# Kernel tuning notes

Hardware: AMD Instinct MI355X
Metric: run time of the kernel (lower is better)

## Reference

```python
import jax, jax.numpy as jnp
import numpy as np

N_NODES = 100000
N_EDGES = 3200000
N_GRAPHS = 64
EPS = 1e-5


def setup_inputs() -> dict:
    key = jax.random.key(0)
    ks = jax.random.split(key, 14)
    x = jax.random.normal(ks[0], (N_NODES, 3), dtype=jnp.float32)
    edge_index = jax.random.randint(ks[1], (2, N_EDGES), 0, N_NODES, dtype=jnp.int32)
    edge_attr = jax.random.uniform(ks[2], (N_EDGES, 2), dtype=jnp.float32)
    batch = jnp.sort(jax.random.randint(ks[3], (N_NODES,), 0, N_GRAPHS, dtype=jnp.int32))
    # SplineConv weights: [K=4 kernels, C_in, C_out]
    W1 = jax.random.normal(ks[4], (4, 3, 8), dtype=jnp.float32) * 0.4
    W2 = jax.random.normal(ks[5], (4, 8, 16), dtype=jnp.float32) * 0.25
    W3 = jax.random.normal(ks[6], (4, 16, 32), dtype=jnp.float32) * 0.2
    g1 = jnp.ones((8,), jnp.float32); b1 = jnp.zeros((8,), jnp.float32)
    g2 = jnp.ones((16,), jnp.float32); b2 = jnp.zeros((16,), jnp.float32)
    g3 = jnp.ones((32,), jnp.float32); b3 = jnp.zeros((32,), jnp.float32)
    fc_w = jax.random.normal(ks[7], (10, 32), dtype=jnp.float32) * 0.15  # Linear(32,10,bias=False)
    return dict(x=x, edge_index=edge_index, edge_attr=edge_attr, batch=batch,
                W1=W1, W2=W2, W3=W3, g1=g1, b1=b1, g2=g2, b2=b2, g3=g3, b3=b3,
                fc_w=fc_w)


def _basis(edge_attr):
    # degree-1 open B-spline, kernel_size=2 per dim, dim=2 -> 4 fixed kernel indices
    u = jnp.clip(edge_attr, 0.0, 1.0)
    u0, u1 = u[:, 0], u[:, 1]
    return jnp.stack([(1 - u0) * (1 - u1),  # kernel (0,0)
                      u0 * (1 - u1),        # kernel (1,0)
                      (1 - u0) * u1,        # kernel (0,1)
                      u0 * u1], axis=-1)    # kernel (1,1)  -> [E,4]


def _spline_conv(x, src, dst, basis, W, inv_deg):
    # gather source feats, basis-weighted kernel mix, scatter-mean to targets
    msg = jnp.einsum('ek,ec,kcd->ed', basis, x[src], W)  # [E, C_out]
    agg = jax.ops.segment_sum(msg, dst, num_segments=x.shape[0])
    return agg * inv_deg


def _bn(x, g, b):
    mu = jnp.mean(x, axis=0)
    var = jnp.mean((x - mu) ** 2, axis=0)  # biased, training-mode BatchNorm
    return (x - mu) * jax.lax.rsqrt(var + EPS) * g + b


def reference(x, edge_index, edge_attr, batch, W1, W2, W3, g1, b1, g2, b2, g3, b3, fc_w):
    src, dst = edge_index[0], edge_index[1]
    B = _basis(edge_attr)
    n = x.shape[0]
    deg = jax.ops.segment_sum(jnp.ones((src.shape[0],), x.dtype), dst, num_segments=n)
    inv_deg = (1.0 / jnp.maximum(deg, 1.0))[:, None]

    h = _bn(jax.nn.elu(_spline_conv(x, src, dst, B, W1, inv_deg)), g1, b1)
    h = _bn(jax.nn.elu(_spline_conv(h, src, dst, B, W2, inv_deg)), g2, b2)
    h = _bn(jax.nn.elu(_spline_conv(h, src, dst, B, W3, inv_deg)), g3, b3)

    pooled = jax.ops.segment_sum(h, batch, num_segments=N_GRAPHS)
    cnt = jax.ops.segment_sum(jnp.ones((n,), h.dtype), batch, num_segments=N_GRAPHS)
    pooled = pooled / jnp.maximum(cnt, 1.0)[:, None]  # global_mean_pool -> [G, 32]
    return pooled @ fc_w.T  # [G, 10]
```

## Files before the change

### kernel.cpp

```cpp
#include <hip/hip_runtime.h>
#include <hip/hip_fp16.h>

#define N_NODES 100000
#define N_EDGES 3200000
#define N_GRAPHS 64
constexpr int NC    = 196;
constexpr int PBLK  = 256;
constexpr int CHUNK = N_EDGES / PBLK;
constexpr int NBLK  = (N_NODES + 255) / 256;
constexpr int LBLK  = N_NODES / 32;
constexpr int FCAP  = 18432;
constexpr int ECAP  = 2048;
#define EPS 1e-5f

typedef float f2 __attribute__((ext_vector_type(2)));
static __device__ __forceinline__ f2 mkf2(float a, float b) { f2 r; r.x = a; r.y = b; return r; }
static __device__ __forceinline__ unsigned h2u(__half2 v) { unsigned r; __builtin_memcpy(&r, &v, 4); return r; }

constexpr size_t OFF_BNS1   = 0x400;
constexpr size_t OFF_BNS2   = 0x500;
constexpr size_t OFF_BNS3   = 0x700;
constexpr size_t OFF_POOLED = 0x1000;
constexpr size_t ZERO_BYTES = 0x3000;
constexpr size_t OFF_CBASE  = 0x4000;
constexpr size_t OFF_BTOT   = 0x5000;
constexpr size_t OFF_ROWPTR = 0x10000;
constexpr size_t OFF_HISTM  = 0x80000;
constexpr size_t OFF_XP     = 0x100000;
constexpr size_t OFF_ES     = 0x200000;
constexpr size_t OFF_EP     = 0x1B00000;
constexpr size_t OFF_T1     = 0x3400000;
constexpr size_t OFF_T2     = 0x3800000;
constexpr size_t OFF_T3     = 0x4000000;

__global__ __launch_bounds__(256) void xpad_kernel(const float* __restrict__ x,
                                                   __half* __restrict__ xp) {
    int n = blockIdx.x * 256 + threadIdx.x;
    if (n >= N_NODES) return;
    __half2 a = __floats2half2_rn(x[n * 3 + 0], x[n * 3 + 1]);
    __half2 b = __floats2half2_rn(x[n * 3 + 2], 0.f);
    *(uint2*)(xp + (size_t)n * 4) = make_uint2(h2u(a), h2u(b));
}

__global__ __launch_bounds__(1024) void k_hist(const int* __restrict__ dst,
                                               int* __restrict__ histM) {
    __shared__ int h[NC];
    for (int i = threadIdx.x; i < NC; i += 1024) h[i] = 0;
    __syncthreads();
    int base = blockIdx.x * CHUNK;
    for (int i = threadIdx.x; i < CHUNK; i += 1024)
        atomicAdd(&h[dst[base + i] >> 9], 1);
    __syncthreads();
    for (int i = threadIdx.x; i < NC; i += 1024)
        histM[i * PBLK + blockIdx.x] = h[i];
}

__global__ __launch_bounds__(256) void k_scan1(int* __restrict__ histM,
                                               int* __restrict__ btot) {
    __shared__ int sd[256];
    int b = blockIdx.x, t = threadIdx.x;
    int v = histM[b * PBLK + t];
    sd[t] = v;
    __syncthreads();
    for (int off = 1; off < 256; off <<= 1) {
        int x = (t >= off) ? sd[t - off] : 0;
        __syncthreads();
        sd[t] += x;
        __syncthreads();
    }
    histM[b * PBLK + t] = sd[t] - v;
    if (t == 255) btot[b] = sd[255];
}

__global__ __launch_bounds__(256) void k_scan2(const int* __restrict__ btot,
                                               int* __restrict__ cbase) {
    __shared__ int sd[256];
    int t = threadIdx.x;
    int v = (t < NC) ? btot[t] : 0;
    sd[t] = v;
    __syncthreads();
    for (int off = 1; off < 256; off <<= 1) {
        int x = (t >= off) ? sd[t - off] : 0;
        __syncthreads();
        sd[t] += x;
        __syncthreads();
    }
    if (t < NC) cbase[t] = sd[t] - v;
    if (t == 0) cbase[NC] = N_EDGES;
}

__global__ __launch_bounds__(1024) void k_part(const int* __restrict__ src,
                                               const int* __restrict__ dst,
                                               const float2* __restrict__ ea,
                                               const int* __restrict__ histM,
                                               const int* __restrict__ cbase,
                                               uint2* __restrict__ Es) {
    __shared__ int cur[NC];
    for (int i = threadIdx.x; i < NC; i += 1024)
        cur[i] = cbase[i] + histM[i * PBLK + blockIdx.x];
    __syncthreads();
    int base = blockIdx.x * CHUNK;
    for (int i = threadIdx.x; i < CHUNK; i += 1024) {
        int e = base + i;
        int d = dst[e];
        float2 u = ea[e];
        float u0 = fminf(fmaxf(u.x, 0.f), 1.f);
        float u1 = fminf(fmaxf(u.y, 0.f), 1.f);
        unsigned u0q = __float2uint_rn(u0 * 524287.f);
        unsigned u1q = __float2uint_rn(u1 * 524287.f);
        unsigned w0 = (unsigned)src[e] | ((u0q & 0x7FFFu) << 17);
        unsigned w1 = (u0q >> 15) | (u1q << 4) | ((unsigned)(d & 511) << 23);
        int pos = atomicAdd(&cur[d >> 9], 1);
        Es[pos] = make_uint2(w0, w1);
    }
}

__global__ __launch_bounds__(1024) void k_fine(const uint2* __restrict__ Es,
                                               const int* __restrict__ cbase,
                                               int* __restrict__ rowptr,
                                               uint2* __restrict__ Ep) {
    extern __shared__ uint2 rec[];
    __shared__ int cnt[512];
    __shared__ int cur[512];
    __shared__ int sd[512];
    int b = blockIdx.x, t = threadIdx.x;
    int lo = cbase[b], hi = cbase[b + 1];
    int m = hi - lo;
    if (t < 512) cnt[t] = 0;
    __syncthreads();
    for (int i = lo + t; i < hi; i += 1024)
        atomicAdd(&cnt[Es[i].y >> 23], 1);
    __syncthreads();
    if (t < 512) sd[t] = cnt[t];
    __syncthreads();
    for (int off = 1; off < 512; off <<= 1) {
        int x = (t < 512 && t >= off) ? sd[t - off] : 0;
        __syncthreads();
        if (t < 512) sd[t] += x;
        __syncthreads();
    }
    if (t < 512) {
        int excl = sd[t] - cnt[t];
        cur[t] = excl;
        int n = b * 512 + t;
        if (n < N_NODES) rowptr[n] = lo + excl;
    }
    if (b == NC - 1 && t == 0) rowptr[N_NODES] = N_EDGES;
    __syncthreads();
    if (m <= FCAP) {
        for (int i = lo + t; i < hi; i += 1024) {
            uint2 r = Es[i];
            int pos = atomicAdd(&cur[r.y >> 23], 1);
            rec[pos] = r;
        }
        __syncthreads();
        for (int i = t; i < m; i += 1024)
            Ep[lo + i] = rec[i];
    } else {
        for (int i = lo + t; i < hi; i += 1024) {
            uint2 r = Es[i];
            int pos = atomicAdd(&cur[r.y >> 23], 1);
            Ep[lo + pos] = r;
        }
    }
}

#define DECODE_EDGE(r)                                              \
    int s = r.x & 0x1FFFF;                                          \
    unsigned u0q = (r.x >> 17) | ((r.y & 0xFu) << 15);              \
    unsigned u1q = (r.y >> 4) & 0x7FFFFu;                           \
    float u0 = u0q * (1.f / 524287.f);                              \
    float u1 = u1q * (1.f / 524287.f);                              \
    float nu0 = 1.f - u0, nu1 = 1.f - u1;                           \
    float b0 = nu0 * nu1, b1 = u0 * nu1, b2 = nu0 * u1, b3 = u0 * u1;

#define L1_BODY                                                     \
        DECODE_EDGE(r)                                              \
        uint2 hv = *(const uint2*)(xp + (size_t)s * 4);             \
        float2 p0 = __half22float2(*(__half2*)&hv.x);               \
        float2 p1 = __half22float2(*(__half2*)&hv.y);               \
        float x0 = p0.x, x1 = p0.y, x2 = p1.x;                      \
        z[0] += b0 * x0; z[1]  += b0 * x1; z[2]  += b0 * x2;        \
        z[3] += b1 * x0; z[4]  += b1 * x1; z[5]  += b1 * x2;        \
        z[6] += b2 * x0; z[7]  += b2 * x1; z[8]  += b2 * x2;        \
        z[9] += b3 * x0; z[10] += b3 * x1; z[11] += b3 * x2;

__global__ __launch_bounds__(256) void layer1_kernel(const __half* __restrict__ xp,
                                                     const int* __restrict__ rowptr,
                                                     const uint2* __restrict__ Ep,
                                                     const float* __restrict__ W,
                                                     __half* __restrict__ tout) {
    __shared__ float Wl[96];
    __shared__ uint2 recL[ECAP];
    for (int i = threadIdx.x; i < 96; i += 256) Wl[i] = W[i];
    int nb = blockIdx.x * 32;
    int eb = rowptr[nb], ee = rowptr[nb + 32];
    int mm = ee - eb;
    if (mm <= ECAP)
        for (int i = threadIdx.x; i < mm; i += 256) recL[i] = Ep[eb + i];
    __syncthreads();
    int lane8 = threadIdx.x & 7;
    int n = nb + (threadIdx.x >> 3);
    int e0 = rowptr[n], e1 = rowptr[n + 1];
    float z[12];
#pragma unroll
    for (int i = 0; i < 12; ++i) z[i] = 0.f;
    if (mm <= ECAP) {
#pragma unroll 4
        for (int j = e0 - eb + lane8, je = e1 - eb; j < je; j += 8) {
            uint2 r = recL[j];
            L1_BODY
        }
    } else {
#pragma unroll 2
        for (int j = e0 + lane8; j < e1; j += 8) {
            uint2 r = Ep[j];
            L1_BODY
        }
    }
#pragma unroll
    for (int i = 0; i < 12; ++i) {
        z[i] += __shfl_xor(z[i], 4);
        z[i] += __shfl_xor(z[i], 2);
        z[i] += __shfl_xor(z[i], 1);
    }
    float y = 0.f;
#pragma unroll
    for (int kc = 0; kc < 12; ++kc) y += z[kc] * Wl[kc * 8 + lane8];
    float invd = 1.f / fmaxf((float)(e1 - e0), 1.f);
    float v = y * invd;
    v = v > 0.f ? v : expm1f(v);
    tout[(size_t)n * 8 + lane8] = __float2half_rn(v);
}

#define L2_BODY                                                     \
        DECODE_EDGE(r)                                              \
        uint2 hv = *(const uint2*)(xin + (size_t)s * 8 + 4 * ch);   \
        float2 p0 = __half22float2(*(__half2*)&hv.x);               \
        float2 p1 = __half22float2(*(__half2*)&hv.y);               \
        f2 x01 = mkf2(p0.x, p0.y), x23 = mkf2(p1.x, p1.y);          \
        S[0] += b0; S[1] += b1; S[2] += b2; S[3] += b3;             \
        f2 bbv;                                                     \
        bbv = mkf2(b0, b0); zf[0] += bbv * x01; zf[1] += bbv * x23; \
        bbv = mkf2(b1, b1); zf[2] += bbv * x01; zf[3] += bbv * x23; \
        bbv = mkf2(b2, b2); zf[4] += bbv * x01; zf[5] += bbv * x23; \
        bbv = mkf2(b3, b3); zf[6] += bbv * x01; zf[7] += bbv * x23;

__global__ __launch_bounds__(256) void layer2_kernel(const __half* __restrict__ xin,
                                                     const float* __restrict__ bns,
                                                     const float* __restrict__ g,
                                                     const float* __restrict__ bb,
                                                     const int* __restrict__ rowptr,
                                                     const uint2* __restrict__ Ep,
                                                     const float* __restrict__ W,
                                                     __half* __restrict__ tout) {
    __shared__ float scA[8], shA[8];
    __shared__ float4 Wl[140];
    __shared__ float shW[64];
    __shared__ uint2 recL[ECAP];
    int t = threadIdx.x;
    if (t < 8) {
        float mu = bns[t] * (1.f / N_NODES);
        float var = fmaxf(bns[8 + t] * (1.f / N_NODES) - mu * mu, 0.f);
        float s = g[t] * rsqrtf(var + EPS);
        scA[t] = s;
        shA[t] = bb[t] - mu * s;
    }
    int nb = blockIdx.x * 32;
    int eb = rowptr[nb], ee = rowptr[nb + 32];
    int mm = ee - eb;
    if (mm <= ECAP)
        for (int i = t; i < mm; i += 256) recL[i] = Ep[eb + i];
    __syncthreads();
    if (t < 128) {
        int k = t >> 5, d4 = (t >> 3) & 3, c = t & 7;
        float4 w = ((const float4*)W)[(k * 8 + c) * 4 + d4];
        float s = scA[c];
        Wl[k * 35 + d4 * 9 + c] = make_float4(w.x * s, w.y * s, w.z * s, w.w * s);
    } else if (t < 192) {
        int j = t - 128;
        int k = j >> 4, d = j & 15;
        float acc = 0.f;
#pragma unroll
        for (int c = 0; c < 8; ++c) acc += shA[c] * W[(k * 8 + c) * 16 + d];
        shW[j] = acc;
    }
    __syncthreads();

    int lane8 = t & 7;
    int kq = lane8 & 3, h = lane8 >> 2;
    int ch = kq & 1;
    int eo = lane8 >> 1;
    int n = nb + (t >> 3);
    int e0 = rowptr[n], e1 = rowptr[n + 1];
    f2 zf[8];
    float S[4];
#pragma unroll
    for (int i = 0; i < 8; ++i) zf[i] = mkf2(0.f, 0.f);
#pragma unroll
    for (int i = 0; i < 4; ++i) S[i] = 0.f;
    if (mm <= ECAP) {
#pragma unroll 4
        for (int j = e0 - eb + eo, je = e1 - eb; j < je; j += 4) {
            uint2 r = recL[j];
            L2_BODY
        }
    } else {
#pragma unroll 2
        for (int j = e0 + eo; j < e1; j += 4) {
            uint2 r = Ep[j];
            L2_BODY
        }
    }
#pragma unroll
    for (int i = 0; i < 8; ++i) {
        zf[i].x += __shfl_xor(zf[i].x, 4); zf[i].y += __shfl_xor(zf[i].y, 4);
        zf[i].x += __shfl_xor(zf[i].x, 2); zf[i].y += __shfl_xor(zf[i].y, 2);
    }
#pragma unroll
    for (int i = 0; i < 4; ++i) { S[i] += __shfl_xor(S[i], 4); S[i] += __shfl_xor(S[i], 2); }

    int laneW = 18 * h + 4 * ch;
    f2 ya[2], yb[2];
#pragma unroll
    for (int i = 0; i < 2; ++i) { ya[i] = mkf2(0.f, 0.f); yb[i] = mkf2(0.f, 0.f); }
#pragma unroll
    for (int k = 0; k < 4; ++k) {
        float zs[4] = {zf[2 * k].x, zf[2 * k].y, zf[2 * k + 1].x, zf[2 * k + 1].y};
#pragma unroll
        for (int i = 0; i < 4; ++i) {
            f2 zsp = mkf2(zs[i], zs[i]);
            int base = k * 35 + i + laneW;
#pragma unroll
            for (int d4 = 0; d4 < 2; ++d4) {
                float4 w = Wl[base + 9 * d4];
                ya[d4] += zsp * mkf2(w.x, w.y);
                yb[d4] += zsp * mkf2(w.z, w.w);
            }
        }
    }
    float y[8];
#pragma unroll
    for (int d4 = 0; d4 < 2; ++d4) {
        y[4 * d4 + 0] = ya[d4].x; y[4 * d4 + 1] = ya[d4].y;
        y[4 * d4 + 2] = yb[d4].x; y[4 * d4 + 3] = yb[d4].y;
    }
    float y1[4];
#pragma unroll
    for (int i = 0; i < 4; ++i) {
        float a = y[i]     + __shfl_xor(y[i],     1);
        float b = y[4 + i] + __shfl_xor(y[4 + i], 1);
        y1[i] = ch ? b : a;
    }
    int qb = (kq >> 1) & 1;
    float f0 = qb ? y1[2] : y1[0];
    float f1 = qb ? y1[3] : y1[1];
    int d = h * 8 + ch * 4 + qb * 2;
    f0 += S[0] * shW[d]     + S[1] * shW[16 + d]     + S[2] * shW[32 + d]     + S[3] * shW[48 + d];
    f1 += S[0] * shW[d + 1] + S[1] * shW[16 + d + 1] + S[2] * shW[32 + d + 1] + S[3] * shW[48 + d + 1];
    float invd = 1.f / fmaxf((float)(e1 - e0), 1.f);
    f0 *= invd; f1 *= invd;
    f0 = f0 > 0.f ? f0 : expm1f(f0);
    f1 = f1 > 0.f ? f1 : expm1f(f1);
    *(__half2*)(tout + (size_t)n * 16 + d) = __floats2half2_rn(f0, f1);
}

#define L3_BODY                                                     \
        DECODE_EDGE(r)                                              \
        uint2 hv = *(const uint2*)(xin + (size_t)s * 16 + 4 * kq);  \
        float2 p0 = __half22float2(*(__half2*)&hv.x);               \
        float2 p1 = __half22float2(*(__half2*)&hv.y);               \
        f2 x01 = mkf2(p0.x, p0.y), x23 = mkf2(p1.x, p1.y);          \
        S[0] += b0; S[1] += b1; S[2] += b2; S[3] += b3;             \
        f2 bbv;                                                     \
        bbv = mkf2(b0, b0); zf[0] += bbv * x01; zf[1] += bbv * x23; \
        bbv = mkf2(b1, b1); zf[2] += bbv * x01; zf[3] += bbv * x23; \
        bbv = mkf2(b2, b2); zf[4] += bbv * x01; zf[5] += bbv * x23; \
        bbv = mkf2(b3, b3); zf[6] += bbv * x01; zf[7] += bbv * x23;

__global__ __launch_bounds__(256) void layer3_kernel(const __half* __restrict__ xin,
                                                     const float* __restrict__ bns,
                                                     const float* __restrict__ g,
                                                     const float* __restrict__ bb,
                                                     const int* __restrict__ rowptr,
                                                     const uint2* __restrict__ Ep,
                                                     const float* __restrict__ W,
                                                     __half* __restrict__ tout) {
    __shared__ float scA[16], shA[16];
    __shared__ float4 Wl[580];
    __shared__ float shW[128];
    __shared__ uint2 recL[ECAP];
    int t = threadIdx.x;
    if (t < 16) {
        float mu = bns[t] * (1.f / N_NODES);
        float var = fmaxf(bns[16 + t] * (1.f / N_NODES) - mu * mu, 0.f);
        float s = g[t] * rsqrtf(var + EPS);
        scA[t] = s;
        shA[t] = bb[t] - mu * s;
    }
    int nb = blockIdx.x * 32;
    int eb = rowptr[nb], ee = rowptr[nb + 32];
    int mm = ee - eb;
    if (mm <= ECAP)
        for (int i = t; i < mm; i += 256) recL[i] = Ep[eb + i];
    __syncthreads();
    for (int i = t; i < 512; i += 256) {
        int k = i >> 7, d4 = (i >> 4) & 7, c = i & 15;
        float4 w = ((const float4*)W)[(k * 16 + c) * 8 + d4];
        float s = scA[c];
        Wl[k * 145 + d4 * 18 + (d4 >> 2) + c + 2 * (c >> 3)] =
            make_float4(w.x * s, w.y * s, w.z * s, w.w * s);
    }
    if (t < 128) {
        int k = t >> 5, d = t & 31;
        float acc = 0.f;
#pragma unroll
        for (int c = 0; c < 16; ++c) acc += shA[c] * W[(k * 16 + c) * 32 + d];
        shW[t] = acc;
    }
    __syncthreads();

    int lane8 = t & 7;
    int kq = lane8 & 3, h = lane8 >> 2;
    int n = nb + (t >> 3);
    int e0 = rowptr[n], e1 = rowptr[n + 1];
    f2 zf[8];
    float S[4];
#pragma unroll
    for (int i = 0; i < 8; ++i) zf[i] = mkf2(0.f, 0.f);
#pragma unroll
    for (int i = 0; i < 4; ++i) S[i] = 0.f;
    if (mm <= ECAP) {
#pragma unroll 4
        for (int j = e0 - eb + h, je = e1 - eb; j < je; j += 2) {
            uint2 r = recL[j];
            L3_BODY
        }
    } else {
#pragma unroll 2
        for (int j = e0 + h; j < e1; j += 2) {
            uint2 r = Ep[j];
            L3_BODY
        }
    }
#pragma unroll
    for (int i = 0; i < 8; ++i) {
        zf[i].x += __shfl_xor(zf[i].x, 4);
        zf[i].y += __shfl_xor(zf[i].y, 4);
    }
#pragma unroll
    for (int i = 0; i < 4; ++i) S[i] += __shfl_xor(S[i], 4);

    int laneW = 4 * kq + 2 * (kq >> 1) + 73 * h;
    f2 ya[4], yb[4];
#pragma unroll
    for (int i = 0; i < 4; ++i) { ya[i] = mkf2(0.f, 0.f); yb[i] = mkf2(0.f, 0.f); }
#pragma unroll
    for (int k = 0; k < 4; ++k) {
        float zs[4] = {zf[2 * k].x, zf[2 * k].y, zf[2 * k + 1].x, zf[2 * k + 1].y};
#pragma unroll
        for (int i = 0; i < 4; ++i) {
            f2 zsp = mkf2(zs[i], zs[i]);
            int base = k * 145 + i + laneW;
#pragma unroll
            for (int d4 = 0; d4 < 4; ++d4) {
                float4 w = Wl[base + 18 * d4];
                ya[d4] += zsp * mkf2(w.x, w.y);
                yb[d4] += zsp * mkf2(w.z, w.w);
            }
        }
    }
    float y[16];
#pragma unroll
    for (int d4 = 0; d4 < 4; ++d4) {
        y[4 * d4 + 0] = ya[d4].x; y[4 * d4 + 1] = ya[d4].y;
        y[4 * d4 + 2] = yb[d4].x; y[4 * d4 + 3] = yb[d4].y;
    }
    float y1[8];
#pragma unroll
    for (int i = 0; i < 8; ++i) {
        float a = y[i]     + __shfl_xor(y[i],     1);
        float b = y[8 + i] + __shfl_xor(y[8 + i], 1);
        y1[i] = (kq & 1) ? b : a;
    }
    float y2[4];
#pragma unroll
    for (int i = 0; i < 4; ++i) {
        float a = y1[i]     + __shfl_xor(y1[i],     2);
        float b = y1[4 + i] + __shfl_xor(y1[4 + i], 2);
        y2[i] = (kq & 2) ? b : a;
    }
    int d = h * 16 + (kq & 1) * 8 + ((kq >> 1) & 1) * 4;
#pragma unroll
    for (int i = 0; i < 4; ++i)
        y2[i] += S[0] * shW[d + i] + S[1] * shW[32 + d + i] +
                 S[2] * shW[64 + d + i] + S[3] * shW[96 + d + i];
    float invd = 1.f / fmaxf((float)(e1 - e0), 1.f);
#pragma unroll
    for (int i = 0; i < 4; ++i) {
        float v = y2[i] * invd;
        y2[i] = v > 0.f ? v : expm1f(v);
    }
    __half2 h01 = __floats2half2_rn(y2[0], y2[1]);
    __half2 h23 = __floats2half2_rn(y2[2], y2[3]);
    uint2 st;
    st.x = h2u(h01);
    st.y = h2u(h23);
    *(uint2*)(tout + (size_t)n * 32 + d) = st;
}

template <int COUT>
__global__ __launch_bounds__(256) void bnstats_kernel(const __half* __restrict__ t,
                                                      float* __restrict__ sums) {
    constexpr int ROWS = 256 / COUT;
    int ch = threadIdx.x % COUT;
    int r = threadIdx.x / COUT;
    float s = 0.f, q = 0.f;
    for (int n = blockIdx.x * ROWS + r; n < N_NODES; n += gridDim.x * ROWS) {
        float v = __half2float(t[(size_t)n * COUT + ch]);
        s += v;
        q += v * v;
    }
    __shared__ float ls[256], lq[256];
    ls[threadIdx.x] = s; lq[threadIdx.x] = q;
    __syncthreads();
    for (int off = 128; off >= COUT; off >>= 1) {
        if (threadIdx.x < off) {
            ls[threadIdx.x] += ls[threadIdx.x + off];
            lq[threadIdx.x] += lq[threadIdx.x + off];
        }
        __syncthreads();
    }
    if (threadIdx.x < COUT) {
        atomicAdd(&sums[ch], ls[threadIdx.x]);
        atomicAdd(&sums[COUT + ch], lq[threadIdx.x]);
    }
}

__global__ __launch_bounds__(256) void pool_kernel(const __half* __restrict__ t3,
                                                   const int* __restrict__ batch,
                                                   float* __restrict__ pooled) {
    __shared__ float tile[256][33];
    __shared__ int lb[256];
    int n = blockIdx.x * 256 + threadIdx.x;
    int valid = N_NODES - blockIdx.x * 256;
    if (valid > 256) valid = 256;
    if (n < N_NODES) {
        const uint4* r = (const uint4*)(t3 + (size_t)n * 32);
#pragma unroll
        for (int i = 0; i < 4; ++i) {
            uint4 v = r[i];
            float2 a = __half22float2(*(__half2*)&v.x);
            float2 b = __half22float2(*(__half2*)&v.y);
            float2 c = __half22float2(*(__half2*)&v.z);
            float2 d = __half22float2(*(__half2*)&v.w);
            tile[threadIdx.x][8 * i + 0] = a.x;
            tile[threadIdx.x][8 * i + 1] = a.y;
            tile[threadIdx.x][8 * i + 2] = b.x;
            tile[threadIdx.x][8 * i + 3] = b.y;
            tile[threadIdx.x][8 * i + 4] = c.x;
            tile[threadIdx.x][8 * i + 5] = c.y;
            tile[threadIdx.x][8 * i + 6] = d.x;
            tile[threadIdx.x][8 * i + 7] = d.y;
        }
        lb[threadIdx.x] = batch[n];
    }
    __syncthreads();
    if (threadIdx.x < 32) {
        int ch = threadIdx.x;
        float run = 0.f;
        int gp = lb[0];
        for (int r = 0; r < valid; ++r) {
            int g = lb[r];
            if (g != gp) {
                atomicAdd(&pooled[gp * 32 + ch], run);
                run = 0.f;
                gp = g;
            }
            run += tile[r][ch];
        }
        atomicAdd(&pooled[gp * 32 + ch], run);
    }
}

__global__ void final_kernel(const float* __restrict__ pooled, const int* __restrict__ batch,
                             const float* __restrict__ bns, const float* __restrict__ g,
                             const float* __restrict__ bb, const float* __restrict__ fcw,
                             float* __restrict__ out) {
    __shared__ float sc3[32], sh3[32];
    __shared__ float rcg[64];
    int t = threadIdx.x;
    if (t < 32) {
        float mu = bns[t] * (1.f / N_NODES);
        float var = fmaxf(bns[32 + t] * (1.f / N_NODES) - mu * mu, 0.f);
        float s = g[t] * rsqrtf(var + EPS);
        sc3[t] = s;
        sh3[t] = bb[t] - mu * s;
    } else if (t >= 64 && t < 128) {
        int gr = t - 64;
        int lo0 = 0, hi0 = N_NODES;
        while (lo0 < hi0) { int m = (lo0 + hi0) >> 1; if (batch[m] < gr) lo0 = m + 1; else hi0 = m; }
        int lo1 = lo0, hi1 = N_NODES;
        while (lo1 < hi1) { int m = (lo1 + hi1) >> 1; if (batch[m] < gr + 1) lo1 = m + 1; else hi1 = m; }
        rcg[gr] = 1.f / fmaxf((float)(lo1 - lo0), 1.f);
    }
    __syncthreads();
    int i = t;
    if (i >= N_GRAPHS * 10) return;
    int gi = i / 10, o = i % 10;
    float rc = rcg[gi];
    float acc = 0.f;
#pragma unroll
    for (int d = 0; d < 32; ++d) {
        float pm = sc3[d] * (pooled[gi * 32 + d] * rc) + sh3[d];
        acc += pm * fcw[o * 32 + d];
    }
    out[i] = acc;
}

extern "C" void kernel_launch(void* const* d_in, const int* in_sizes, int n_in,
                              void* d_out, int out_size, void* d_ws, size_t ws_size,
                              hipStream_t stream) {
    const float* x   = (const float*)d_in[0];
    const int*   ei  = (const int*)d_in[1];
    const float* ea  = (const float*)d_in[2];
    const int*   bat = (const int*)d_in[3];
    const float* W1  = (const float*)d_in[4];
    const float* W2  = (const float*)d_in[5];
    const float* W3  = (const float*)d_in[6];
    const float* g1  = (const float*)d_in[7];
    const float* b1  = (const float*)d_in[8];
    const float* g2  = (const float*)d_in[9];
    const float* b2  = (const float*)d_in[10];
    const float* g3  = (const float*)d_in[11];
    const float* b3  = (const float*)d_in[12];
    const float* fcw = (const float*)d_in[13];
    float* out = (float*)d_out;
    char* ws = (char*)d_ws;

    float*  bns1   = (float*)(ws + OFF_BNS1);
    float*  bns2   = (float*)(ws + OFF_BNS2);
    float*  bns3   = (float*)(ws + OFF_BNS3);
    float*  pooled = (float*)(ws + OFF_POOLED);
    int*    cbase  = (int*)(ws + OFF_CBASE);
    int*    btot   = (int*)(ws + OFF_BTOT);
    int*    rowptr = (int*)(ws + OFF_ROWPTR);
    int*    histM  = (int*)(ws + OFF_HISTM);
    uint2*  Es     = (uint2*)(ws + OFF_ES);
    uint2*  Ep     = (uint2*)(ws + OFF_EP);
    __half* xp     = (__half*)(ws + OFF_XP);
    __half* t1     = (__half*)(ws + OFF_T1);
    __half* t2     = (__half*)(ws + OFF_T2);
    __half* t3     = (__half*)(ws + OFF_T3);

    const int* src = ei;
    const int* dst = ei + N_EDGES;

    hipFuncSetAttribute((const void*)k_fine,
                        hipFuncAttributeMaxDynamicSharedMemorySize, FCAP * 8);

    hipMemsetAsync(ws, 0, ZERO_BYTES, stream);

    xpad_kernel<<<NBLK, 256, 0, stream>>>(x, xp);
    k_hist<<<PBLK, 1024, 0, stream>>>(dst, histM);
    k_scan1<<<NC, 256, 0, stream>>>(histM, btot);
    k_scan2<<<1, 256, 0, stream>>>(btot, cbase);
    k_part<<<PBLK, 1024, 0, stream>>>(src, dst, (const float2*)ea, histM, cbase, Es);
    k_fine<<<NC, 1024, FCAP * 8, stream>>>(Es, cbase, rowptr, Ep);

    layer1_kernel<<<LBLK, 256, 0, stream>>>(xp, rowptr, Ep, W1, t1);
    bnstats_kernel<8><<<256, 256, 0, stream>>>(t1, bns1);

    layer2_kernel<<<LBLK, 256, 0, stream>>>(t1, bns1, g1, b1, rowptr, Ep, W2, t2);
    bnstats_kernel<16><<<256, 256, 0, stream>>>(t2, bns2);

    layer3_kernel<<<LBLK, 256, 0, stream>>>(t2, bns2, g2, b2, rowptr, Ep, W3, t3);
    bnstats_kernel<32><<<256, 256, 0, stream>>>(t3, bns3);

    pool_kernel<<<NBLK, 256, 0, stream>>>(t3, bat, pooled);
    final_kernel<<<1, 640, 0, stream>>>(pooled, bat, bns3, g3, b3, fcw, out);
}
```

Measured before the change: 203.1 us.

## Stage partitioned edges in shared memory before coalesced bucket writes

The coarse partition kernel now builds a local histogram of each block's chunk, scans it, and scatters packed edge records into shared memory grouped by bucket. Each wavefront then copies whole bucket runs to global memory contiguously. This replaces random 8-byte global scatter writes with coalesced ones. In exchange it re-reads dst, adds extra syncs and scans, and needs 100 KB of dynamic LDS per block (CHUNK*8), which limits occupancy to one block per CU.

New measurement: 197.1 us. 3.0% less time.

```diff
diff --git a/kernel.cpp b/kernel.cpp
--- a/kernel.cpp
+++ b/kernel.cpp
@@ -95,12 +95,37 @@
                                                const int* __restrict__ histM,
                                                const int* __restrict__ cbase,
                                                uint2* __restrict__ Es) {
+    extern __shared__ uint2 rec[];
+    __shared__ int cnt[NC];
     __shared__ int cur[NC];
-    for (int i = threadIdx.x; i < NC; i += 1024)
-        cur[i] = cbase[i] + histM[i * PBLK + blockIdx.x];
-    __syncthreads();
-    int base = blockIdx.x * CHUNK;
-    for (int i = threadIdx.x; i < CHUNK; i += 1024) {
+    __shared__ int lst[NC];
+    __shared__ int gof[NC];
+    __shared__ int sd[256];
+    int t = threadIdx.x, b = blockIdx.x;
+    for (int i = t; i < NC; i += 1024) cnt[i] = 0;
+    __syncthreads();
+    int base = b * CHUNK;
+    for (int i = t; i < CHUNK; i += 1024)
+        atomicAdd(&cnt[dst[base + i] >> 9], 1);
+    __syncthreads();
+    int v = 0;
+    if (t < 256) { v = (t < NC) ? cnt[t] : 0; sd[t] = v; }
+    __syncthreads();
+    for (int off = 1; off < 256; off <<= 1) {
+        int x = 0;
+        if (t < 256 && t >= off) x = sd[t - off];
+        __syncthreads();
+        if (t < 256) sd[t] += x;
+        __syncthreads();
+    }
+    if (t < NC) {
+        int excl = sd[t] - v;
+        cur[t] = excl;
+        lst[t] = excl;
+        gof[t] = cbase[t] + histM[t * PBLK + b];
+    }
+    __syncthreads();
+    for (int i = t; i < CHUNK; i += 1024) {
         int e = base + i;
         int d = dst[e];
         float2 u = ea[e];
@@ -111,7 +136,16 @@
         unsigned w0 = (unsigned)src[e] | ((u0q & 0x7FFFu) << 17);
         unsigned w1 = (u0q >> 15) | (u1q << 4) | ((unsigned)(d & 511) << 23);
         int pos = atomicAdd(&cur[d >> 9], 1);
-        Es[pos] = make_uint2(w0, w1);
+        rec[pos] = make_uint2(w0, w1);
+    }
+    __syncthreads();
+    int wave = t >> 6, lane = t & 63;
+    for (int bk = wave; bk < NC; bk += 16) {
+        int ls = lst[bk];
+        int len = cnt[bk];
+        int gs = gof[bk];
+        for (int i = lane; i < len; i += 64)
+            Es[gs + i] = rec[ls + i];
     }
 }
 
@@ -658,6 +692,8 @@
 
     hipFuncSetAttribute((const void*)k_fine,
                         hipFuncAttributeMaxDynamicSharedMemorySize, FCAP * 8);
+    hipFuncSetAttribute((const void*)k_part,
+                        hipFuncAttributeMaxDynamicSharedMemorySize, CHUNK * 8);
 
     hipMemsetAsync(ws, 0, ZERO_BYTES, stream);
 
@@ -665,7 +701,7 @@
     k_hist<<<PBLK, 1024, 0, stream>>>(dst, histM);
     k_scan1<<<NC, 256, 0, stream>>>(histM, btot);
     k_scan2<<<1, 256, 0, stream>>>(btot, cbase);
-    k_part<<<PBLK, 1024, 0, stream>>>(src, dst, (const float2*)ea, histM, cbase, Es);
+    k_part<<<PBLK, 1024, CHUNK * 8, stream>>>(src, dst, (const float2*)ea, histM, cbase, Es);
     k_fine<<<NC, 1024, FCAP * 8, stream>>>(Es, cbase, rowptr, Ep);
 
     layer1_kernel<<<LBLK, 256, 0, stream>>>(xp, rowptr, Ep, W1, t1);
```
